# Optimization experiments

Hardware: AMD Instinct MI355X
Metric: run time of the kernel (lower is better)

Reference implementation:

```python
import jax, jax.numpy as jnp
import numpy as np

BT = 64  # chunk size (BLOCK_SIZE_C)
EPS = 1e-06


def setup_inputs() -> dict:
    key = jax.random.key(0)
    k1, k2, k3, k4 = jax.random.split(key, 4)
    B, H, S, D = 4, 8, 4096, 128
    q = jax.random.normal(k1, (B, H, S, D), dtype=jnp.float32)
    k = jax.random.normal(k2, (B, H, S, D), dtype=jnp.float32)
    v = jax.random.normal(k3, (B, H, S, D), dtype=jnp.float32)
    beta = jax.random.uniform(k4, (B, H, S), dtype=jnp.float32)
    return {"q": q, "k": k, "v": v, "beta": beta}


def _chunk_gated_delta_fwd(q, k, v, beta):
    # Recurrence: S_t = beta_t * S_{t-1} + k_t (x) v_t ;  o_t = q_t @ S_t
    B, H, S, D = q.shape
    NC = S // BT
    f32 = jnp.float32
    qf = q.astype(f32).reshape(B, H, NC, BT, D)
    kf = k.astype(f32).reshape(B, H, NC, BT, D)
    vf = v.astype(f32).reshape(B, H, NC, BT, D)
    log_beta = jnp.log(beta.astype(f32).reshape(B, H, NC, BT) + EPS)
    cum = jnp.cumsum(log_beta, axis=-1)                     # [B,H,NC,BT]
    tot = cum[..., -1]                                      # [B,H,NC]
    decay_from_start = jnp.exp(cum)                         # [B,H,NC,BT]
    decay_to_end = jnp.exp(tot[..., None] - cum)            # [B,H,NC,BT]
    causal = jnp.tril(jnp.ones((BT, BT), dtype=bool))
    decay_matrix = jnp.exp(cum[..., :, None] - cum[..., None, :])  # [B,H,NC,BT,BT]
    decay_masked = jnp.where(causal, decay_matrix, 0.0)
    # intra-chunk contribution (fully parallel across chunks)
    qk = jnp.einsum('bhcid,bhcjd->bhcij', qf, kf)
    out_intra = jnp.einsum('bhcij,bhcjd->bhcid', qk * decay_masked, vf)
    # per-chunk state-update term: (k * decay_to_end)^T @ v
    upd = jnp.einsum('bhcid,bhcie->bhcde', kf * decay_to_end[..., None], vf)
    # sequential inter-chunk recurrence over chunks
    def step(state, xs):
        qc, dfs_c, tot_c, upd_c = xs
        out_inter = jnp.einsum('bhid,bhde->bhie', qc * dfs_c[..., None], state)
        new_state = state * jnp.exp(tot_c)[..., None, None] + upd_c
        return new_state, out_inter
    xs = (jnp.moveaxis(qf, 2, 0), jnp.moveaxis(decay_from_start, 2, 0),
          jnp.moveaxis(tot, 2, 0), jnp.moveaxis(upd, 2, 0))
    state0 = jnp.zeros((B, H, D, D), dtype=f32)
    _, out_inter = jax.lax.scan(step, state0, xs)           # [NC,B,H,BT,D]
    out = out_intra + jnp.moveaxis(out_inter, 0, 2)
    return out.reshape(B, H, S, D).astype(q.dtype)


def reference(q, k, v, beta):
    return _chunk_gated_delta_fwd(q, k, v, beta)
```

## Files before the change

### kernel.cpp

```cpp
#include <hip/hip_runtime.h>
#include <hip/hip_bf16.h>
#include <math.h>

#define Gp  32
#define Sp  4096
#define Dp  128
#define BTp 64
#define NCp 64

typedef __attribute__((ext_vector_type(8))) short bf16x8;
typedef __attribute__((ext_vector_type(4))) float f32x4;

#define MFMA(a,b,c) __builtin_amdgcn_mfma_f32_16x16x32_bf16((a),(b),(c),0,0,0)

#define STR 72

__device__ inline unsigned pack2(float lo, float hi) {
    __hip_bfloat162 h = __float22bfloat162_rn(make_float2(lo, hi));
    union { __hip_bfloat162 v; unsigned u; } t; t.v = h; return t.u;
}
__device__ inline float bflo(unsigned u) { union { unsigned u; float f; } t; t.u = u << 16; return t.f; }
__device__ inline float bfhi(unsigned u) { union { unsigned u; float f; } t; t.u = u & 0xffff0000u; return t.f; }

__global__ __launch_bounds__(256, 4) void gdn_intra(
    const float* __restrict__ q, const float* __restrict__ k,
    const float* __restrict__ v, const float* __restrict__ beta,
    float* __restrict__ out, unsigned short* __restrict__ upd,
    float* __restrict__ tot_buf, float* __restrict__ dfs_buf)
{
    __shared__ unsigned short s_vt[128 * STR];
    __shared__ unsigned short s_kt[128 * STR];

    const int blk = blockIdx.x, g = blk >> 6, c = blk & 63;
    const int tid = threadIdx.x, lane = tid & 63, w = tid >> 6;
    const int m16 = lane & 15, quad = lane >> 4;
    const size_t base  = ((size_t)g * Sp + (size_t)c * BTp) * Dp;
    const size_t bbase = (size_t)g * Sp + (size_t)c * BTp;

    float x = logf(beta[bbase + lane] + 1e-6f);
    #pragma unroll
    for (int off = 1; off < 64; off <<= 1) {
        float n = __shfl_up(x, off, 64);
        if (lane >= off) x += n;
    }
    const float tot = __shfl(x, 63, 64);
    const float dte_own = expf(tot - x);
    if (tid < 64) dfs_buf[bbase + lane] = expf(x);
    if (tid == 63) tot_buf[g * NCp + c] = tot;

    #pragma unroll
    for (int it = 0; it < 8; ++it) {
        const int u = it * 256 + tid;
        const int d = (u & 63) * 2, i = (u >> 6) * 2;
        const float dte0 = __shfl(dte_own, i, 64);
        const float dte1 = __shfl(dte_own, i + 1, 64);
        const float2 va = *(const float2*)(v + base + (size_t)i * Dp + d);
        const float2 vb = *(const float2*)(v + base + (size_t)(i + 1) * Dp + d);
        const float2 ka = *(const float2*)(k + base + (size_t)i * Dp + d);
        const float2 kb = *(const float2*)(k + base + (size_t)(i + 1) * Dp + d);
        *(unsigned*)&s_vt[d * STR + i]       = pack2(va.x, vb.x);
        *(unsigned*)&s_vt[(d + 1) * STR + i] = pack2(va.y, vb.y);
        *(unsigned*)&s_kt[d * STR + i]       = pack2(ka.x * dte0, kb.x * dte1);
        *(unsigned*)&s_kt[(d + 1) * STR + i] = pack2(ka.y * dte0, kb.y * dte1);
    }

    bf16x8 qf[4];
    {
        const float* qrow = q + base + (size_t)(16 * w + m16) * Dp + quad * 8;
        #pragma unroll
        for (int ks = 0; ks < 4; ++ks) {
            const float4 a = *(const float4*)(qrow + ks * 32);
            const float4 b = *(const float4*)(qrow + ks * 32 + 4);
            union { bf16x8 v; unsigned ui[4]; } t;
            t.ui[0] = pack2(a.x, a.y); t.ui[1] = pack2(a.z, a.w);
            t.ui[2] = pack2(b.x, b.y); t.ui[3] = pack2(b.z, b.w);
            qf[ks] = t.v;
        }
    }

    f32x4 accP[4] = {};
    #pragma unroll
    for (int nt = 0; nt < 4; ++nt) {
        if (nt <= w) {
            const float* krow = k + base + (size_t)(16 * nt + m16) * Dp + quad * 8;
            float4 ra[4], rb[4];
            #pragma unroll
            for (int ks = 0; ks < 4; ++ks) {
                ra[ks] = *(const float4*)(krow + ks * 32);
                rb[ks] = *(const float4*)(krow + ks * 32 + 4);
            }
            #pragma unroll
            for (int ks = 0; ks < 4; ++ks) {
                union { bf16x8 v; unsigned ui[4]; } t;
                t.ui[0] = pack2(ra[ks].x, ra[ks].y); t.ui[1] = pack2(ra[ks].z, ra[ks].w);
                t.ui[2] = pack2(rb[ks].x, rb[ks].y); t.ui[3] = pack2(rb[ks].z, rb[ks].w);
                accP[nt] = MFMA(t.v, qf[ks], accP[nt]);
            }
        }
    }

    const float ci = __shfl(x, 16 * w + m16, 64);
    unsigned p_pk[4][2];
    #pragma unroll
    for (int nt = 0; nt < 4; ++nt) { p_pk[nt][0] = 0u; p_pk[nt][1] = 0u; }
    #pragma unroll
    for (int nt = 0; nt < 4; ++nt) {
        if (nt <= w) {
            float pm[4];
            #pragma unroll
            for (int r = 0; r < 4; ++r) {
                const int j = 16 * nt + 4 * quad + r;
                const float cj = __shfl(x, j, 64);
                float val = accP[nt][r] * expf(ci - cj);
                if (nt == w) val = (16 * w + m16 >= j) ? val : 0.f;
                pm[r] = val;
            }
            p_pk[nt][0] = pack2(pm[0], pm[1]);
            p_pk[nt][1] = pack2(pm[2], pm[3]);
        }
    }

    bf16x8 af[2];
    #pragma unroll
    for (int ks = 0; ks < 2; ++ks) {
        if (ks <= (w >> 1)) {
            union { bf16x8 v; unsigned ui[4]; } t;
            #pragma unroll
            for (int m = 0; m < 4; ++m) {
                const int src = m16 + 16 * (2 * (quad & 1) + (m >> 1));
                const unsigned aA = (unsigned)__shfl((int)p_pk[2 * ks][m & 1], src, 64);
                const unsigned aB = (unsigned)__shfl((int)p_pk[2 * ks + 1][m & 1], src, 64);
                t.ui[m] = (quad >> 1) ? aB : aA;
            }
            af[ks] = t.v;
        }
    }

    __syncthreads();

    {
        f32x4 accU[2][8] = {};
        #pragma unroll
        for (int ks = 0; ks < 2; ++ks) {
            const bf16x8 b0 = *(const bf16x8*)&s_vt[(16 * (2 * w)     + m16) * STR + quad * 8 + ks * 32];
            const bf16x8 b1 = *(const bf16x8*)&s_vt[(16 * (2 * w + 1) + m16) * STR + quad * 8 + ks * 32];
            #pragma unroll
            for (int nt = 0; nt < 8; ++nt) {
                const bf16x8 a = *(const bf16x8*)&s_kt[(16 * nt + m16) * STR + quad * 8 + ks * 32];
                accU[0][nt] = MFMA(a, b0, accU[0][nt]);
                accU[1][nt] = MFMA(a, b1, accU[1][nt]);
            }
        }
        unsigned short* ub = upd + (size_t)blk * Dp * Dp;
        #pragma unroll
        for (int mt = 0; mt < 2; ++mt) {
            const int e = 16 * (2 * w + mt) + m16;
            #pragma unroll
            for (int nt = 0; nt < 8; ++nt) {
                uint2 pw;
                pw.x = pack2(accU[mt][nt][0], accU[mt][nt][1]);
                pw.y = pack2(accU[mt][nt][2], accU[mt][nt][3]);
                *(uint2*)&ub[(size_t)e * Dp + 16 * nt + 4 * quad] = pw;
            }
        }
    }

    {
        f32x4 accO[8] = {};
        #pragma unroll
        for (int ks = 0; ks < 2; ++ks) {
            if (ks <= (w >> 1)) {
                #pragma unroll
                for (int nt = 0; nt < 8; ++nt) {
                    const bf16x8 a = *(const bf16x8*)&s_vt[(16 * nt + m16) * STR + quad * 8 + ks * 32];
                    accO[nt] = MFMA(a, af[ks], accO[nt]);
                }
            }
        }
        const int i = 16 * w + m16;
        #pragma unroll
        for (int nt = 0; nt < 8; ++nt) {
            float4 st;
            st.x = accO[nt][0]; st.y = accO[nt][1];
            st.z = accO[nt][2]; st.w = accO[nt][3];
            *(float4*)&out[base + (size_t)i * Dp + 16 * nt + 4 * quad] = st;
        }
    }
}

__global__ __launch_bounds__(128) void gdn_scan(
    unsigned short* __restrict__ upd, const float* __restrict__ tot_buf)
{
    const int g = blockIdx.x >> 4, slab = blockIdx.x & 15, tid = threadIdx.x;
    __shared__ float s_e[NCp];
    if (tid < NCp) s_e[tid] = expf(tot_buf[g * NCp + tid]);
    __syncthreads();
    uint4* b = (uint4*)(upd + (size_t)g * NCp * Dp * Dp) + slab * 128 + tid;
    float s0 = 0.f, s1 = 0.f, s2 = 0.f, s3 = 0.f;
    float s4 = 0.f, s5 = 0.f, s6 = 0.f, s7 = 0.f;
    uint4 pf[4];
    #pragma unroll
    for (int j = 0; j < 4; ++j) pf[j] = b[(size_t)j * 2048];
    #pragma unroll
    for (int cc = 0; cc < NCp; ++cc) {
        const uint4 cur = pf[cc & 3];
        if (cc + 4 < NCp) pf[cc & 3] = b[(size_t)(cc + 4) * 2048];
        const float e = s_e[cc];
        uint4 stq;
        stq.x = pack2(s0, s1); stq.y = pack2(s2, s3);
        stq.z = pack2(s4, s5); stq.w = pack2(s6, s7);
        b[(size_t)cc * 2048] = stq;
        s0 = s0 * e + bflo(cur.x); s1 = s1 * e + bfhi(cur.x);
        s2 = s2 * e + bflo(cur.y); s3 = s3 * e + bfhi(cur.y);
        s4 = s4 * e + bflo(cur.z); s5 = s5 * e + bfhi(cur.z);
        s6 = s6 * e + bflo(cur.w); s7 = s7 * e + bfhi(cur.w);
    }
}

__global__ __launch_bounds__(256) void gdn_inter(
    const float* __restrict__ q, const unsigned short* __restrict__ state,
    const float* __restrict__ dfs_buf, float* __restrict__ out)
{
    const int blk = blockIdx.x, g = blk >> 6, c = blk & 63;
    const int tid = threadIdx.x, lane = tid & 63, w = tid >> 6;
    const int m16 = lane & 15, quad = lane >> 4;
    const size_t base  = ((size_t)g * Sp + (size_t)c * BTp) * Dp;
    const size_t bbase = (size_t)g * Sp + (size_t)c * BTp;
    const unsigned short* sb = state + (size_t)blk * Dp * Dp;
    const int i0 = 16 * w + quad * 4;

    const float scale = dfs_buf[bbase + 16 * w + m16];
    bf16x8 qf[4];
    const float* qrow = q + base + (size_t)(16 * w + m16) * Dp + quad * 8;
    #pragma unroll
    for (int ks = 0; ks < 4; ++ks) {
        const float4 a = *(const float4*)(qrow + ks * 32);
        const float4 b = *(const float4*)(qrow + ks * 32 + 4);
        union { bf16x8 v; unsigned ui[4]; } t;
        t.ui[0] = pack2(a.x * scale, a.y * scale);
        t.ui[1] = pack2(a.z * scale, a.w * scale);
        t.ui[2] = pack2(b.x * scale, b.y * scale);
        t.ui[3] = pack2(b.w * scale, b.w * scale);
        t.ui[3] = pack2(b.z * scale, b.w * scale);
        qf[ks] = t.v;
    }

    float ov[8][4];
    #pragma unroll
    for (int nt = 0; nt < 8; ++nt)
        #pragma unroll
        for (int r = 0; r < 4; ++r)
            ov[nt][r] = out[base + (size_t)(i0 + r) * Dp + 16 * nt + m16];

    f32x4 acc[8] = {};
    #pragma unroll
    for (int ks = 0; ks < 4; ++ks) {
        bf16x8 bfr[8];
        #pragma unroll
        for (int nt = 0; nt < 8; ++nt)
            bfr[nt] = *(const bf16x8*)(sb + (16 * nt + m16) * Dp + quad * 8 + ks * 32);
        #pragma unroll
        for (int nt = 0; nt < 8; ++nt)
            acc[nt] = MFMA(qf[ks], bfr[nt], acc[nt]);
    }
    #pragma unroll
    for (int nt = 0; nt < 8; ++nt) {
        const int e = 16 * nt + m16;
        #pragma unroll
        for (int r = 0; r < 4; ++r)
            out[base + (size_t)(i0 + r) * Dp + e] = ov[nt][r] + acc[nt][r];
    }
}

extern "C" void kernel_launch(void* const* d_in, const int* in_sizes, int n_in,
                              void* d_out, int out_size, void* d_ws, size_t ws_size,
                              hipStream_t stream) {
    const float* q    = (const float*)d_in[0];
    const float* k    = (const float*)d_in[1];
    const float* v    = (const float*)d_in[2];
    const float* beta = (const float*)d_in[3];
    float* out = (float*)d_out;

    unsigned short* upd = (unsigned short*)d_ws;
    float* tot_buf = (float*)(upd + (size_t)Gp * NCp * Dp * Dp);
    float* dfs_buf = tot_buf + Gp * NCp;

    gdn_intra<<<Gp * NCp, 256, 0, stream>>>(q, k, v, beta, out, upd, tot_buf, dfs_buf);
    gdn_scan <<<Gp * 16, 128, 0, stream>>>(upd, tot_buf);
    gdn_inter<<<Gp * NCp, 256, 0, stream>>>(q, upd, dfs_buf, out);
}
```

Measured before the change: 320.7 us.

## Stage K in swizzled LDS, vectorize transposes, and make inter-kernel output I/O row-contiguous

The intra kernel now loads K once into an XOR-swizzled bf16 LDS tile for the QK^T MFMA instead of re-reading fp32 K rows from global memory per tile. The V/K transposes use 8-row register gathers and 128-bit swizzled LDS stores instead of padded 32-bit stores. The inter kernel swaps MFMA operand order so each lane holds four contiguous output columns, turning scalar strided read-modify-write of out into float4 accesses. The extra LDS buffer raises shared memory use and the occupancy hint drops from 4 to 3 blocks per CU.

New measurement: 315.6 us. No clear change (-1.6%).

```diff
diff --git a/kernel.cpp b/kernel.cpp
--- a/kernel.cpp
+++ b/kernel.cpp
@@ -13,7 +13,7 @@
 
 #define MFMA(a,b,c) __builtin_amdgcn_mfma_f32_16x16x32_bf16((a),(b),(c),0,0,0)
 
-#define STR 72
+#define TSWZ(d, slot) ((((slot) ^ (((d) & 15) >> 1)) << 3))
 
 __device__ inline unsigned pack2(float lo, float hi) {
     __hip_bfloat162 h = __float22bfloat162_rn(make_float2(lo, hi));
@@ -22,14 +22,15 @@
 __device__ inline float bflo(unsigned u) { union { unsigned u; float f; } t; t.u = u << 16; return t.f; }
 __device__ inline float bfhi(unsigned u) { union { unsigned u; float f; } t; t.u = u & 0xffff0000u; return t.f; }
 
-__global__ __launch_bounds__(256, 4) void gdn_intra(
+__global__ __launch_bounds__(256, 3) void gdn_intra(
     const float* __restrict__ q, const float* __restrict__ k,
     const float* __restrict__ v, const float* __restrict__ beta,
     float* __restrict__ out, unsigned short* __restrict__ upd,
     float* __restrict__ tot_buf, float* __restrict__ dfs_buf)
 {
-    __shared__ unsigned short s_vt[128 * STR];
-    __shared__ unsigned short s_kt[128 * STR];
+    __shared__ unsigned short s_k [64 * 128];
+    __shared__ unsigned short s_vt[128 * 64];
+    __shared__ unsigned short s_kt[128 * 64];
 
     const int blk = blockIdx.x, g = blk >> 6, c = blk & 63;
     const int tid = threadIdx.x, lane = tid & 63, w = tid >> 6;
@@ -47,22 +48,6 @@
     const float dte_own = expf(tot - x);
     if (tid < 64) dfs_buf[bbase + lane] = expf(x);
     if (tid == 63) tot_buf[g * NCp + c] = tot;
-
-    #pragma unroll
-    for (int it = 0; it < 8; ++it) {
-        const int u = it * 256 + tid;
-        const int d = (u & 63) * 2, i = (u >> 6) * 2;
-        const float dte0 = __shfl(dte_own, i, 64);
-        const float dte1 = __shfl(dte_own, i + 1, 64);
-        const float2 va = *(const float2*)(v + base + (size_t)i * Dp + d);
-        const float2 vb = *(const float2*)(v + base + (size_t)(i + 1) * Dp + d);
-        const float2 ka = *(const float2*)(k + base + (size_t)i * Dp + d);
-        const float2 kb = *(const float2*)(k + base + (size_t)(i + 1) * Dp + d);
-        *(unsigned*)&s_vt[d * STR + i]       = pack2(va.x, vb.x);
-        *(unsigned*)&s_vt[(d + 1) * STR + i] = pack2(va.y, vb.y);
-        *(unsigned*)&s_kt[d * STR + i]       = pack2(ka.x * dte0, kb.x * dte1);
-        *(unsigned*)&s_kt[(d + 1) * STR + i] = pack2(ka.y * dte0, kb.y * dte1);
-    }
 
     bf16x8 qf[4];
     {
@@ -78,23 +63,55 @@
         }
     }
 
+    #pragma unroll
+    for (int it = 0; it < 8; ++it) {
+        const int idx = (it * 256 + tid) * 4;
+        const int i = idx >> 7, d = idx & 127;
+        const float4 kv = *(const float4*)(k + base + (size_t)i * Dp + d);
+        const int ad = i * 128 + (((d >> 3) ^ (i & 15)) << 3) + (d & 7);
+        uint2 pw; pw.x = pack2(kv.x, kv.y); pw.y = pack2(kv.z, kv.w);
+        *(uint2*)&s_k[ad] = pw;
+    }
+
+    #pragma unroll
+    for (int it = 0; it < 2; ++it) {
+        const int dd = 2 * (tid & 63);
+        const int i  = 32 * it + 8 * w;
+        float2 lv[8], lk[8];
+        #pragma unroll
+        for (int r = 0; r < 8; ++r) {
+            lv[r] = *(const float2*)(v + base + (size_t)(i + r) * Dp + dd);
+            lk[r] = *(const float2*)(k + base + (size_t)(i + r) * Dp + dd);
+        }
+        float dt[8];
+        #pragma unroll
+        for (int r = 0; r < 8; ++r) dt[r] = __shfl(dte_own, i + r, 64);
+        const int sl = TSWZ(dd, i >> 3);
+        uint4 t0, t1;
+        t0.x = pack2(lv[0].x, lv[1].x); t0.y = pack2(lv[2].x, lv[3].x);
+        t0.z = pack2(lv[4].x, lv[5].x); t0.w = pack2(lv[6].x, lv[7].x);
+        t1.x = pack2(lv[0].y, lv[1].y); t1.y = pack2(lv[2].y, lv[3].y);
+        t1.z = pack2(lv[4].y, lv[5].y); t1.w = pack2(lv[6].y, lv[7].y);
+        *(uint4*)&s_vt[dd * 64 + sl]       = t0;
+        *(uint4*)&s_vt[(dd + 1) * 64 + sl] = t1;
+        t0.x = pack2(lk[0].x * dt[0], lk[1].x * dt[1]); t0.y = pack2(lk[2].x * dt[2], lk[3].x * dt[3]);
+        t0.z = pack2(lk[4].x * dt[4], lk[5].x * dt[5]); t0.w = pack2(lk[6].x * dt[6], lk[7].x * dt[7]);
+        t1.x = pack2(lk[0].y * dt[0], lk[1].y * dt[1]); t1.y = pack2(lk[2].y * dt[2], lk[3].y * dt[3]);
+        t1.z = pack2(lk[4].y * dt[4], lk[5].y * dt[5]); t1.w = pack2(lk[6].y * dt[6], lk[7].y * dt[7]);
+        *(uint4*)&s_kt[dd * 64 + sl]       = t0;
+        *(uint4*)&s_kt[(dd + 1) * 64 + sl] = t1;
+    }
+
+    __syncthreads();
+
     f32x4 accP[4] = {};
     #pragma unroll
     for (int nt = 0; nt < 4; ++nt) {
         if (nt <= w) {
-            const float* krow = k + base + (size_t)(16 * nt + m16) * Dp + quad * 8;
-            float4 ra[4], rb[4];
             #pragma unroll
             for (int ks = 0; ks < 4; ++ks) {
-                ra[ks] = *(const float4*)(krow + ks * 32);
-                rb[ks] = *(const float4*)(krow + ks * 32 + 4);
-            }
-            #pragma unroll
-            for (int ks = 0; ks < 4; ++ks) {
-                union { bf16x8 v; unsigned ui[4]; } t;
-                t.ui[0] = pack2(ra[ks].x, ra[ks].y); t.ui[1] = pack2(ra[ks].z, ra[ks].w);
-                t.ui[2] = pack2(rb[ks].x, rb[ks].y); t.ui[3] = pack2(rb[ks].z, rb[ks].w);
-                accP[nt] = MFMA(t.v, qf[ks], accP[nt]);
+                const bf16x8 kf = *(const bf16x8*)&s_k[(16 * nt + m16) * 128 + (((quad + 4 * ks) ^ m16) << 3)];
+                accP[nt] = MFMA(kf, qf[ks], accP[nt]);
             }
         }
     }
@@ -136,17 +153,16 @@
         }
     }
 
-    __syncthreads();
-
     {
         f32x4 accU[2][8] = {};
         #pragma unroll
         for (int ks = 0; ks < 2; ++ks) {
-            const bf16x8 b0 = *(const bf16x8*)&s_vt[(16 * (2 * w)     + m16) * STR + quad * 8 + ks * 32];
-            const bf16x8 b1 = *(const bf16x8*)&s_vt[(16 * (2 * w + 1) + m16) * STR + quad * 8 + ks * 32];
+            const int sw = TSWZ(m16, quad + 4 * ks);
+            const bf16x8 b0 = *(const bf16x8*)&s_vt[(16 * (2 * w)     + m16) * 64 + sw];
+            const bf16x8 b1 = *(const bf16x8*)&s_vt[(16 * (2 * w + 1) + m16) * 64 + sw];
             #pragma unroll
             for (int nt = 0; nt < 8; ++nt) {
-                const bf16x8 a = *(const bf16x8*)&s_kt[(16 * nt + m16) * STR + quad * 8 + ks * 32];
+                const bf16x8 a = *(const bf16x8*)&s_kt[(16 * nt + m16) * 64 + sw];
                 accU[0][nt] = MFMA(a, b0, accU[0][nt]);
                 accU[1][nt] = MFMA(a, b1, accU[1][nt]);
             }
@@ -170,9 +186,10 @@
         #pragma unroll
         for (int ks = 0; ks < 2; ++ks) {
             if (ks <= (w >> 1)) {
+                const int sw = TSWZ(m16, quad + 4 * ks);
                 #pragma unroll
                 for (int nt = 0; nt < 8; ++nt) {
-                    const bf16x8 a = *(const bf16x8*)&s_vt[(16 * nt + m16) * STR + quad * 8 + ks * 32];
+                    const bf16x8 a = *(const bf16x8*)&s_vt[(16 * nt + m16) * 64 + sw];
                     accO[nt] = MFMA(a, af[ks], accO[nt]);
                 }
             }
@@ -227,11 +244,11 @@
     const size_t base  = ((size_t)g * Sp + (size_t)c * BTp) * Dp;
     const size_t bbase = (size_t)g * Sp + (size_t)c * BTp;
     const unsigned short* sb = state + (size_t)blk * Dp * Dp;
-    const int i0 = 16 * w + quad * 4;
-
-    const float scale = dfs_buf[bbase + 16 * w + m16];
+    const int i = 16 * w + m16;
+
+    const float scale = dfs_buf[bbase + i];
     bf16x8 qf[4];
-    const float* qrow = q + base + (size_t)(16 * w + m16) * Dp + quad * 8;
+    const float* qrow = q + base + (size_t)i * Dp + quad * 8;
     #pragma unroll
     for (int ks = 0; ks < 4; ++ks) {
         const float4 a = *(const float4*)(qrow + ks * 32);
@@ -240,35 +257,32 @@
         t.ui[0] = pack2(a.x * scale, a.y * scale);
         t.ui[1] = pack2(a.z * scale, a.w * scale);
         t.ui[2] = pack2(b.x * scale, b.y * scale);
-        t.ui[3] = pack2(b.w * scale, b.w * scale);
         t.ui[3] = pack2(b.z * scale, b.w * scale);
         qf[ks] = t.v;
     }
 
-    float ov[8][4];
+    float4 ov[8];
     #pragma unroll
     for (int nt = 0; nt < 8; ++nt)
-        #pragma unroll
-        for (int r = 0; r < 4; ++r)
-            ov[nt][r] = out[base + (size_t)(i0 + r) * Dp + 16 * nt + m16];
+        ov[nt] = *(const float4*)&out[base + (size_t)i * Dp + 16 * nt + 4 * quad];
 
     f32x4 acc[8] = {};
     #pragma unroll
     for (int ks = 0; ks < 4; ++ks) {
-        bf16x8 bfr[8];
+        bf16x8 afr[8];
         #pragma unroll
         for (int nt = 0; nt < 8; ++nt)
-            bfr[nt] = *(const bf16x8*)(sb + (16 * nt + m16) * Dp + quad * 8 + ks * 32);
+            afr[nt] = *(const bf16x8*)(sb + (16 * nt + m16) * Dp + quad * 8 + ks * 32);
         #pragma unroll
         for (int nt = 0; nt < 8; ++nt)
-            acc[nt] = MFMA(qf[ks], bfr[nt], acc[nt]);
+            acc[nt] = MFMA(afr[nt], qf[ks], acc[nt]);
     }
     #pragma unroll
     for (int nt = 0; nt < 8; ++nt) {
-        const int e = 16 * nt + m16;
-        #pragma unroll
-        for (int r = 0; r < 4; ++r)
-            out[base + (size_t)(i0 + r) * Dp + e] = ov[nt][r] + acc[nt][r];
+        float4 st;
+        st.x = ov[nt].x + acc[nt][0]; st.y = ov[nt].y + acc[nt][1];
+        st.z = ov[nt].z + acc[nt][2]; st.w = ov[nt].w + acc[nt][3];
+        *(float4*)&out[base + (size_t)i * Dp + 16 * nt + 4 * quad] = st;
     }
 }
 
```
